# Performance work log

Measured on AMD Instinct MI355X. Metric: run time of the kernel, lower is better.

The kernel has to match this reference:

```python
import jax, jax.numpy as jnp
import numpy as np

B, C, H, W, IC = 8, 128, 64, 32, 64
NEG = -9.0e15  # matches torch's -9000000000000000.0 mask value


def setup_inputs() -> dict:
    key = jax.random.key(0)
    ks = jax.random.split(key, 8)
    x = jax.random.normal(ks[0], (B, C, H, W), dtype=jnp.float32)
    adj = jax.random.randint(ks[1], (H * W, H * W), 0, 2, dtype=jnp.int32)
    s = 0.1  # keep pre-softmax logits in a sane range
    g_w = jax.random.normal(ks[2], (IC, C), dtype=jnp.float32) * s
    theta_w = jax.random.normal(ks[3], (IC, C), dtype=jnp.float32) * s
    phi_w = jax.random.normal(ks[4], (IC, C), dtype=jnp.float32) * s
    cp_w = jax.random.normal(ks[5], (2 * IC,), dtype=jnp.float32) * s
    g_b = jnp.zeros((IC,), jnp.float32)
    theta_b = jnp.zeros((IC,), jnp.float32)
    phi_b = jnp.zeros((IC,), jnp.float32)
    return {"x": x, "adj": adj, "g_w": g_w, "g_b": g_b, "theta_w": theta_w,
            "theta_b": theta_b, "phi_w": phi_w, "phi_b": phi_b, "cp_w": cp_w}


def reference(x, adj, g_w, g_b, theta_w, theta_b, phi_w, phi_b, cp_w):
    b, c, h, w = x.shape
    n = h * w
    ic = g_w.shape[0]
    xf = x.reshape(b, c, n)  # flatten spatial sites: (B,C,N)
    # 1x1 convs == per-site linear projections
    g_x = jnp.einsum('oc,bcn->bno', g_w, xf) + g_b          # (B,N,IC)
    th = jnp.einsum('oc,bcn->bon', theta_w, xf) + theta_b[:, None]  # (B,IC,N)
    ph = jnp.einsum('oc,bcn->bon', phi_w, xf) + phi_b[:, None]      # (B,IC,N)
    # concat_project 1x1 conv on [theta;phi] channels == broadcast sum of two dot products
    w_t, w_p = cp_w[:ic], cp_w[ic:]
    f_t = jnp.einsum('o,bon->bn', w_t, th)  # (B,N)
    f_p = jnp.einsum('o,bon->bn', w_p, ph)  # (B,N)
    e = jax.nn.leaky_relu(f_t[:, :, None] + f_p[:, None, :], 0.2)  # (B,N,N)
    attention = jnp.where(adj > 0, jnp.float32(NEG), e)
    attention = jax.nn.softmax(attention, axis=-1)
    y = jnp.einsum('bij,bjo->bio', attention, g_x)  # (B,N,IC)
    return y.transpose(0, 2, 1).reshape(b, ic, h, w)
```

## Files before the change

### kernel.cpp

```cpp
#include <hip/hip_runtime.h>
#include <hip/hip_bf16.h>
#include <cstdint>

#define B_    8
#define C_    128
#define IC_   64
#define N_    2048
#define ROWS  16
#define LOG2E 1.44269504088896340736f

typedef __attribute__((ext_vector_type(8))) short bf16x8;
typedef __attribute__((ext_vector_type(4))) float f32x4;

#define OFF_FT   0
#define OFF_FP   16384
#define OFF_GXB  32768

static __device__ __forceinline__ ushort f2bf(float f) {
  __hip_bfloat16 h = __float2bfloat16(f);
  return *reinterpret_cast<ushort*>(&h);
}

__global__ __launch_bounds__(256) void k_gx(const float* __restrict__ x,
                                            const float* __restrict__ g_w,
                                            const float* __restrict__ g_b,
                                            const float* __restrict__ theta_w,
                                            const float* __restrict__ theta_b,
                                            const float* __restrict__ phi_w,
                                            const float* __restrict__ phi_b,
                                            const float* __restrict__ cp_w,
                                            float* __restrict__ ws) {
  __shared__ float xs[C_][64];
  __shared__ float wgT[C_][IC_];
  __shared__ float vtp[2][C_];
  __shared__ float fred[2][4][64];
  __shared__ float fb[2];
  int bx = blockIdx.x;
  int b = bx >> 5, n0 = (bx & 31) * 64;
  int t = threadIdx.x;

  const float* xb = x + (size_t)b * C_ * N_ + n0;
  for (int idx = t; idx < C_ * 64; idx += 256) {
    int c = idx >> 6, n = idx & 63;
    xs[c][n] = xb[(size_t)c * N_ + n];
  }
  for (int idx = t; idx < C_ * IC_; idx += 256) {
    int c = idx >> 6, o = idx & 63;
    wgT[c][o] = g_w[o * C_ + c];
  }
  {
    int half = t >> 7;
    int c = t & 127;
    const float* wmat = half ? phi_w : theta_w;
    const float* cw = cp_w + half * IC_;
    float a = 0.f;
#pragma unroll 8
    for (int o = 0; o < IC_; ++o) a += cw[o] * wmat[o * C_ + c];
    vtp[half][c] = a * LOG2E;
  }
  if (t < 2) {
    const float* bv = t ? phi_b : theta_b;
    const float* cw = cp_w + t * IC_;
    float a = 0.f;
    for (int o = 0; o < IC_; ++o) a += cw[o] * bv[o];
    fb[t] = a * LOG2E;
  }
  __syncthreads();

  int o4 = (t & 15) * 4, n4 = (t >> 4) * 4;
  float acc[4][4] = {};
#pragma unroll 4
  for (int c = 0; c < C_; ++c) {
    float4 xv = *(const float4*)&xs[c][n4];
    float4 wv = *(const float4*)&wgT[c][o4];
    acc[0][0] += wv.x * xv.x; acc[0][1] += wv.x * xv.y; acc[0][2] += wv.x * xv.z; acc[0][3] += wv.x * xv.w;
    acc[1][0] += wv.y * xv.x; acc[1][1] += wv.y * xv.y; acc[1][2] += wv.y * xv.z; acc[1][3] += wv.y * xv.w;
    acc[2][0] += wv.z * xv.x; acc[2][1] += wv.z * xv.y; acc[2][2] += wv.z * xv.z; acc[2][3] += wv.z * xv.w;
    acc[3][0] += wv.w * xv.x; acc[3][1] += wv.w * xv.y; acc[3][2] += wv.w * xv.z; acc[3][3] += wv.w * xv.w;
  }
  __hip_bfloat16* gxT = (__hip_bfloat16*)(ws + OFF_GXB) + (size_t)b * IC_ * N_;
#pragma unroll
  for (int oo = 0; oo < 4; ++oo) {
    float gb = g_b[o4 + oo];
    ushort4 pk = make_ushort4(f2bf(acc[oo][0] + gb), f2bf(acc[oo][1] + gb),
                              f2bf(acc[oo][2] + gb), f2bf(acc[oo][3] + gb));
    *(ushort4*)(gxT + (size_t)(o4 + oo) * N_ + n0 + n4) = pk;
  }

  {
    int n = t & 63, qr = t >> 6;
    float ft = 0.f, fp = 0.f;
#pragma unroll 8
    for (int cc = 0; cc < 32; ++cc) {
      int c = qr * 32 + cc;
      float xv = xs[c][n];
      ft += xv * vtp[0][c];
      fp += xv * vtp[1][c];
    }
    fred[0][qr][n] = ft;
    fred[1][qr][n] = fp;
  }
  __syncthreads();
  if (t < 128) {
    int n = t & 63, isp = t >> 6;
    float f = fb[isp] + fred[isp][0][n] + fred[isp][1][n]
            + fred[isp][2][n] + fred[isp][3][n];
    ws[(isp ? OFF_FP : OFF_FT) + b * N_ + n0 + n] = f;
  }
}

__global__ __launch_bounds__(256) void k_attn(const int* __restrict__ adj,
                                              const float* __restrict__ ws,
                                              float* __restrict__ out) {
  __shared__ char pbuf[2][ROWS * 512 * 2];
  __shared__ float rowsum[ROWS];

  int bx = blockIdx.x;
  int b = bx >> 7, tile = bx & 127;
  int i0 = tile * ROWS;
  int t = threadIdx.x;
  int w = t >> 6, lane = t & 63;
  int c16 = lane & 15, agrp = lane >> 4;

  const float* f_t = ws + OFF_FT + b * N_;
  const float4* fp4 = (const float4*)(ws + OFF_FP + b * N_);
  const __hip_bfloat16* gxT = (const __hip_bfloat16*)(ws + OFF_GXB) + (size_t)b * IC_ * N_;
  const __hip_bfloat16* gwav = gxT + (size_t)(w * 16 + c16) * N_ + agrp * 8;

  float fti[4];
#pragma unroll
  for (int rr = 0; rr < 4; ++rr) fti[rr] = f_t[i0 + w * 4 + rr];

  float rs[4] = {0.f, 0.f, 0.f, 0.f};
  f32x4 acc = {0.f, 0.f, 0.f, 0.f};

  for (int ch = 0; ch < 4; ++ch) {
    int j0 = ch * 512;
    char* pb = pbuf[ch & 1];
    float4 fa = fp4[j0 / 4 + lane * 2];
    float4 fbv = fp4[j0 / 4 + lane * 2 + 1];
#pragma unroll
    for (int rr = 0; rr < 4; ++rr) {
      int r = w * 4 + rr;
      const int4* ap = (const int4*)(adj + (size_t)(i0 + r) * N_ + j0) + lane * 2;
      int4 a0 = ap[0], a1 = ap[1];
      float ft = fti[rr];
      float s0 = ft + fa.x;  s0 = fmaxf(s0, 0.2f * s0);
      float s1 = ft + fa.y;  s1 = fmaxf(s1, 0.2f * s1);
      float s2 = ft + fa.z;  s2 = fmaxf(s2, 0.2f * s2);
      float s3 = ft + fa.w;  s3 = fmaxf(s3, 0.2f * s3);
      float s4 = ft + fbv.x; s4 = fmaxf(s4, 0.2f * s4);
      float s5 = ft + fbv.y; s5 = fmaxf(s5, 0.2f * s5);
      float s6 = ft + fbv.z; s6 = fmaxf(s6, 0.2f * s6);
      float s7 = ft + fbv.w; s7 = fmaxf(s7, 0.2f * s7);
      float p0 = (a0.x > 0) ? 0.f : exp2f(s0);
      float p1 = (a0.y > 0) ? 0.f : exp2f(s1);
      float p2 = (a0.z > 0) ? 0.f : exp2f(s2);
      float p3 = (a0.w > 0) ? 0.f : exp2f(s3);
      float p4 = (a1.x > 0) ? 0.f : exp2f(s4);
      float p5 = (a1.y > 0) ? 0.f : exp2f(s5);
      float p6 = (a1.z > 0) ? 0.f : exp2f(s6);
      float p7 = (a1.w > 0) ? 0.f : exp2f(s7);
      rs[rr] += ((p0 + p1) + (p2 + p3)) + ((p4 + p5) + (p6 + p7));
      bf16x8 pk;
      pk[0] = (short)f2bf(p0); pk[1] = (short)f2bf(p1);
      pk[2] = (short)f2bf(p2); pk[3] = (short)f2bf(p3);
      pk[4] = (short)f2bf(p4); pk[5] = (short)f2bf(p5);
      pk[6] = (short)f2bf(p6); pk[7] = (short)f2bf(p7);
      size_t byte = ((size_t)r * 1024 + (size_t)lane * 16) ^ ((size_t)(r & 7) << 4);
      *(bf16x8*)(pb + byte) = pk;
    }
    __syncthreads();
#pragma unroll
    for (int ks = 0; ks < 16; ++ks) {
      size_t ab = ((size_t)c16 * 1024 + (size_t)ks * 64 + (size_t)agrp * 16)
                ^ ((size_t)(c16 & 7) << 4);
      bf16x8 af = *(const bf16x8*)(pb + ab);
      bf16x8 bf = *(const bf16x8*)(gwav + j0 + ks * 32);
      acc = __builtin_amdgcn_mfma_f32_16x16x32_bf16(af, bf, acc, 0, 0, 0);
    }
  }

#pragma unroll
  for (int rr = 0; rr < 4; ++rr) {
    float s = rs[rr];
#pragma unroll
    for (int off = 32; off; off >>= 1) s += __shfl_xor(s, off, 64);
    if (lane == 0) rowsum[w * 4 + rr] = s;
  }
  __syncthreads();

  float4 rsv = *(const float4*)&rowsum[agrp * 4];
  float* op = out + ((size_t)b * IC_ + w * 16 + c16) * N_ + i0 + agrp * 4;
  float4 res = make_float4(acc[0] / rsv.x, acc[1] / rsv.y,
                           acc[2] / rsv.z, acc[3] / rsv.w);
  *(float4*)op = res;
}

extern "C" void kernel_launch(void* const* d_in, const int* in_sizes, int n_in,
                              void* d_out, int out_size, void* d_ws, size_t ws_size,
                              hipStream_t stream) {
  const float* x       = (const float*)d_in[0];
  const int*   adj     = (const int*)  d_in[1];
  const float* g_w     = (const float*)d_in[2];
  const float* g_b     = (const float*)d_in[3];
  const float* theta_w = (const float*)d_in[4];
  const float* theta_b = (const float*)d_in[5];
  const float* phi_w   = (const float*)d_in[6];
  const float* phi_b   = (const float*)d_in[7];
  const float* cp_w    = (const float*)d_in[8];
  float* out = (float*)d_out;
  float* ws  = (float*)d_ws;

  k_gx<<<B_ * (N_ / 64), 256, 0, stream>>>(x, g_w, g_b, theta_w, theta_b,
                                           phi_w, phi_b, cp_w, ws);
  k_attn<<<B_ * (N_ / ROWS), 256, 0, stream>>>(adj, ws, out);
}
```

Before: 133.6 us.

## Build attention MFMA operand in registers and retile rows per wave

```diff
diff --git a/kernel.cpp b/kernel.cpp
--- a/kernel.cpp
+++ b/kernel.cpp
@@ -6,7 +6,6 @@
 #define C_    128
 #define IC_   64
 #define N_    2048
-#define ROWS  16
 #define LOG2E 1.44269504088896340736f
 
 typedef __attribute__((ext_vector_type(8))) short bf16x8;
@@ -109,92 +108,80 @@
   }
 }
 
-__global__ __launch_bounds__(256) void k_attn(const int* __restrict__ adj,
-                                              const float* __restrict__ ws,
-                                              float* __restrict__ out) {
-  __shared__ char pbuf[2][ROWS * 512 * 2];
-  __shared__ float rowsum[ROWS];
-
+__global__ __launch_bounds__(256, 2) void k_attn(const int* __restrict__ adj,
+                                                 const float* __restrict__ ws,
+                                                 float* __restrict__ out) {
   int bx = blockIdx.x;
-  int b = bx >> 7, tile = bx & 127;
-  int i0 = tile * ROWS;
+  int b = bx >> 6, st = bx & 63;
   int t = threadIdx.x;
   int w = t >> 6, lane = t & 63;
-  int c16 = lane & 15, agrp = lane >> 4;
+  int col = lane & 15, agrp = lane >> 4;
+  int rowbase = st * 32 + (w >> 1) * 16;
+  int obase = (w & 1) * 32;
 
   const float* f_t = ws + OFF_FT + b * N_;
-  const float4* fp4 = (const float4*)(ws + OFF_FP + b * N_);
+  const float4* fpv = (const float4*)(ws + OFF_FP + b * N_);
   const __hip_bfloat16* gxT = (const __hip_bfloat16*)(ws + OFF_GXB) + (size_t)b * IC_ * N_;
-  const __hip_bfloat16* gwav = gxT + (size_t)(w * 16 + c16) * N_ + agrp * 8;
-
-  float fti[4];
-#pragma unroll
-  for (int rr = 0; rr < 4; ++rr) fti[rr] = f_t[i0 + w * 4 + rr];
-
-  float rs[4] = {0.f, 0.f, 0.f, 0.f};
-  f32x4 acc = {0.f, 0.f, 0.f, 0.f};
-
-  for (int ch = 0; ch < 4; ++ch) {
-    int j0 = ch * 512;
-    char* pb = pbuf[ch & 1];
-    float4 fa = fp4[j0 / 4 + lane * 2];
-    float4 fbv = fp4[j0 / 4 + lane * 2 + 1];
-#pragma unroll
-    for (int rr = 0; rr < 4; ++rr) {
-      int r = w * 4 + rr;
-      const int4* ap = (const int4*)(adj + (size_t)(i0 + r) * N_ + j0) + lane * 2;
-      int4 a0 = ap[0], a1 = ap[1];
-      float ft = fti[rr];
-      float s0 = ft + fa.x;  s0 = fmaxf(s0, 0.2f * s0);
-      float s1 = ft + fa.y;  s1 = fmaxf(s1, 0.2f * s1);
-      float s2 = ft + fa.z;  s2 = fmaxf(s2, 0.2f * s2);
-      float s3 = ft + fa.w;  s3 = fmaxf(s3, 0.2f * s3);
-      float s4 = ft + fbv.x; s4 = fmaxf(s4, 0.2f * s4);
-      float s5 = ft + fbv.y; s5 = fmaxf(s5, 0.2f * s5);
-      float s6 = ft + fbv.z; s6 = fmaxf(s6, 0.2f * s6);
-      float s7 = ft + fbv.w; s7 = fmaxf(s7, 0.2f * s7);
-      float p0 = (a0.x > 0) ? 0.f : exp2f(s0);
-      float p1 = (a0.y > 0) ? 0.f : exp2f(s1);
-      float p2 = (a0.z > 0) ? 0.f : exp2f(s2);
-      float p3 = (a0.w > 0) ? 0.f : exp2f(s3);
-      float p4 = (a1.x > 0) ? 0.f : exp2f(s4);
-      float p5 = (a1.y > 0) ? 0.f : exp2f(s5);
-      float p6 = (a1.z > 0) ? 0.f : exp2f(s6);
-      float p7 = (a1.w > 0) ? 0.f : exp2f(s7);
-      rs[rr] += ((p0 + p1) + (p2 + p3)) + ((p4 + p5) + (p6 + p7));
-      bf16x8 pk;
-      pk[0] = (short)f2bf(p0); pk[1] = (short)f2bf(p1);
-      pk[2] = (short)f2bf(p2); pk[3] = (short)f2bf(p3);
-      pk[4] = (short)f2bf(p4); pk[5] = (short)f2bf(p5);
-      pk[6] = (short)f2bf(p6); pk[7] = (short)f2bf(p7);
-      size_t byte = ((size_t)r * 1024 + (size_t)lane * 16) ^ ((size_t)(r & 7) << 4);
-      *(bf16x8*)(pb + byte) = pk;
-    }
-    __syncthreads();
-#pragma unroll
-    for (int ks = 0; ks < 16; ++ks) {
-      size_t ab = ((size_t)c16 * 1024 + (size_t)ks * 64 + (size_t)agrp * 16)
-                ^ ((size_t)(c16 & 7) << 4);
-      bf16x8 af = *(const bf16x8*)(pb + ab);
-      bf16x8 bf = *(const bf16x8*)(gwav + j0 + ks * 32);
-      acc = __builtin_amdgcn_mfma_f32_16x16x32_bf16(af, bf, acc, 0, 0, 0);
-    }
-  }
-
-#pragma unroll
-  for (int rr = 0; rr < 4; ++rr) {
-    float s = rs[rr];
-#pragma unroll
-    for (int off = 32; off; off >>= 1) s += __shfl_xor(s, off, 64);
-    if (lane == 0) rowsum[w * 4 + rr] = s;
-  }
-  __syncthreads();
-
-  float4 rsv = *(const float4*)&rowsum[agrp * 4];
-  float* op = out + ((size_t)b * IC_ + w * 16 + c16) * N_ + i0 + agrp * 4;
-  float4 res = make_float4(acc[0] / rsv.x, acc[1] / rsv.y,
-                           acc[2] / rsv.z, acc[3] / rsv.w);
-  *(float4*)op = res;
+  const __hip_bfloat16* gw0 = gxT + (size_t)(obase + col) * N_ + agrp * 8;
+  const __hip_bfloat16* gw1 = gw0 + 16 * N_;
+
+  float fti = f_t[rowbase + col];
+  const int4*   arow = (const int4*)(adj + (size_t)(rowbase + col) * N_) + agrp * 2;
+  const float4* fpl  = fpv + agrp * 2;
+
+  f32x4 acc0 = {0.f, 0.f, 0.f, 0.f};
+  f32x4 acc1 = {0.f, 0.f, 0.f, 0.f};
+  float rsum = 0.f;
+
+#pragma unroll 2
+  for (int ks = 0; ks < 64; ++ks) {
+    int4   a0 = arow[ks * 8];
+    int4   a1 = arow[ks * 8 + 1];
+    float4 f0 = fpl[ks * 8];
+    float4 f1 = fpl[ks * 8 + 1];
+    bf16x8 b0 = *(const bf16x8*)(gw0 + ks * 32);
+    bf16x8 b1 = *(const bf16x8*)(gw1 + ks * 32);
+
+    float s0 = fti + f0.x; s0 = fmaxf(s0, 0.2f * s0);
+    float s1 = fti + f0.y; s1 = fmaxf(s1, 0.2f * s1);
+    float s2 = fti + f0.z; s2 = fmaxf(s2, 0.2f * s2);
+    float s3 = fti + f0.w; s3 = fmaxf(s3, 0.2f * s3);
+    float s4 = fti + f1.x; s4 = fmaxf(s4, 0.2f * s4);
+    float s5 = fti + f1.y; s5 = fmaxf(s5, 0.2f * s5);
+    float s6 = fti + f1.z; s6 = fmaxf(s6, 0.2f * s6);
+    float s7 = fti + f1.w; s7 = fmaxf(s7, 0.2f * s7);
+    float p0 = (a0.x > 0) ? 0.f : exp2f(s0);
+    float p1 = (a0.y > 0) ? 0.f : exp2f(s1);
+    float p2 = (a0.z > 0) ? 0.f : exp2f(s2);
+    float p3 = (a0.w > 0) ? 0.f : exp2f(s3);
+    float p4 = (a1.x > 0) ? 0.f : exp2f(s4);
+    float p5 = (a1.y > 0) ? 0.f : exp2f(s5);
+    float p6 = (a1.z > 0) ? 0.f : exp2f(s6);
+    float p7 = (a1.w > 0) ? 0.f : exp2f(s7);
+    rsum += ((p0 + p1) + (p2 + p3)) + ((p4 + p5) + (p6 + p7));
+
+    bf16x8 af;
+    af[0] = (short)f2bf(p0); af[1] = (short)f2bf(p1);
+    af[2] = (short)f2bf(p2); af[3] = (short)f2bf(p3);
+    af[4] = (short)f2bf(p4); af[5] = (short)f2bf(p5);
+    af[6] = (short)f2bf(p6); af[7] = (short)f2bf(p7);
+
+    acc0 = __builtin_amdgcn_mfma_f32_16x16x32_bf16(af, b0, acc0, 0, 0, 0);
+    acc1 = __builtin_amdgcn_mfma_f32_16x16x32_bf16(af, b1, acc1, 0, 0, 0);
+  }
+
+  rsum += __shfl_xor(rsum, 16, 64);
+  rsum += __shfl_xor(rsum, 32, 64);
+  float r0 = __shfl(rsum, agrp * 4 + 0, 64);
+  float r1 = __shfl(rsum, agrp * 4 + 1, 64);
+  float r2 = __shfl(rsum, agrp * 4 + 2, 64);
+  float r3 = __shfl(rsum, agrp * 4 + 3, 64);
+
+  float4 res0 = make_float4(acc0[0] / r0, acc0[1] / r1, acc0[2] / r2, acc0[3] / r3);
+  float4 res1 = make_float4(acc1[0] / r0, acc1[1] / r1, acc1[2] / r2, acc1[3] / r3);
+  float* op = out + ((size_t)b * IC_ + obase + col) * N_ + rowbase + agrp * 4;
+  *(float4*)op             = res0;
+  *(float4*)(op + 16 * N_) = res1;
 }
 
 extern "C" void kernel_launch(void* const* d_in, const int* in_sizes, int n_in,
@@ -214,5 +201,5 @@
 
   k_gx<<<B_ * (N_ / 64), 256, 0, stream>>>(x, g_w, g_b, theta_w, theta_b,
                                            phi_w, phi_b, cp_w, ws);
-  k_attn<<<B_ * (N_ / ROWS), 256, 0, stream>>>(adj, ws, out);
-}
+  k_attn<<<B_ * (N_ / 32), 256, 0, stream>>>(adj, ws, out);
+}
```

Result: slower. 162.0 us (+21.2%).

## Split attention key range across waves with register prefetch and barrier-free LDS staging

Applied to the files above, without the earlier changes.

```diff
diff --git a/kernel.cpp b/kernel.cpp
--- a/kernel.cpp
+++ b/kernel.cpp
@@ -6,7 +6,6 @@
 #define C_    128
 #define IC_   64
 #define N_    2048
-#define ROWS  16
 #define LOG2E 1.44269504088896340736f
 
 typedef __attribute__((ext_vector_type(8))) short bf16x8;
@@ -109,92 +108,134 @@
   }
 }
 
-__global__ __launch_bounds__(256) void k_attn(const int* __restrict__ adj,
-                                              const float* __restrict__ ws,
-                                              float* __restrict__ out) {
-  __shared__ char pbuf[2][ROWS * 512 * 2];
-  __shared__ float rowsum[ROWS];
+__global__ __launch_bounds__(128, 2) void k_attn(const int* __restrict__ adj,
+                                                 const float* __restrict__ ws,
+                                                 float* __restrict__ out) {
+  __shared__ char pstage[2][2][2048];
+  __shared__ float mrg[64][20];
+  __shared__ float rsm[16];
 
   int bx = blockIdx.x;
-  int b = bx >> 7, tile = bx & 127;
-  int i0 = tile * ROWS;
+  int b = bx >> 7, rt = bx & 127;
+  int rowbase = rt * 16;
   int t = threadIdx.x;
-  int w = t >> 6, lane = t & 63;
-  int c16 = lane & 15, agrp = lane >> 4;
+  int wid = t >> 6, lane = t & 63;
+  int c16 = lane & 15, g8 = lane >> 4;
+  int jbase = wid * 1024;
 
   const float* f_t = ws + OFF_FT + b * N_;
-  const float4* fp4 = (const float4*)(ws + OFF_FP + b * N_);
+  const float* f_p = ws + OFF_FP + b * N_ + jbase + c16 * 4;
   const __hip_bfloat16* gxT = (const __hip_bfloat16*)(ws + OFF_GXB) + (size_t)b * IC_ * N_;
-  const __hip_bfloat16* gwav = gxT + (size_t)(w * 16 + c16) * N_ + agrp * 8;
 
   float fti[4];
 #pragma unroll
-  for (int rr = 0; rr < 4; ++rr) fti[rr] = f_t[i0 + w * 4 + rr];
-
-  float rs[4] = {0.f, 0.f, 0.f, 0.f};
-  f32x4 acc = {0.f, 0.f, 0.f, 0.f};
-
-  for (int ch = 0; ch < 4; ++ch) {
-    int j0 = ch * 512;
-    char* pb = pbuf[ch & 1];
-    float4 fa = fp4[j0 / 4 + lane * 2];
-    float4 fbv = fp4[j0 / 4 + lane * 2 + 1];
+  for (int rr = 0; rr < 4; ++rr) fti[rr] = f_t[rowbase + rr * 4 + g8];
+
+  const int* arow0 = adj + (size_t)(rowbase + g8) * N_ + jbase + c16 * 4;
+  const __hip_bfloat16* gw0 = gxT + (size_t)c16 * N_ + jbase + g8 * 8;
+
+  int4 ca[4]; float4 cf; bf16x8 cg[8];
+#pragma unroll
+  for (int rr = 0; rr < 4; ++rr) ca[rr] = *(const int4*)(arow0 + (size_t)rr * 4 * N_);
+  cf = *(const float4*)(f_p);
+#pragma unroll
+  for (int ot = 0; ot < 4; ++ot) {
+    cg[ot * 2 + 0] = *(const bf16x8*)(gw0 + (size_t)ot * 16 * N_);
+    cg[ot * 2 + 1] = *(const bf16x8*)(gw0 + (size_t)ot * 16 * N_ + 32);
+  }
+
+  f32x4 acc[4];
+#pragma unroll
+  for (int ot = 0; ot < 4; ++ot) acc[ot] = (f32x4){0.f, 0.f, 0.f, 0.f};
+  float rsum[4] = {0.f, 0.f, 0.f, 0.f};
+
+  for (int w = 0; w < 16; ++w) {
+    int nw = (w < 15) ? w + 1 : 15;
+    int4 na[4]; float4 nf; bf16x8 ng[8];
+#pragma unroll
+    for (int rr = 0; rr < 4; ++rr)
+      na[rr] = *(const int4*)(arow0 + (size_t)rr * 4 * N_ + nw * 64);
+    nf = *(const float4*)(f_p + nw * 64);
+#pragma unroll
+    for (int ot = 0; ot < 4; ++ot) {
+      ng[ot * 2 + 0] = *(const bf16x8*)(gw0 + (size_t)ot * 16 * N_ + nw * 64);
+      ng[ot * 2 + 1] = *(const bf16x8*)(gw0 + (size_t)ot * 16 * N_ + nw * 64 + 32);
+    }
+
+    char* pb = pstage[wid][w & 1];
 #pragma unroll
     for (int rr = 0; rr < 4; ++rr) {
-      int r = w * 4 + rr;
-      const int4* ap = (const int4*)(adj + (size_t)(i0 + r) * N_ + j0) + lane * 2;
-      int4 a0 = ap[0], a1 = ap[1];
+      int4 a = ca[rr];
       float ft = fti[rr];
-      float s0 = ft + fa.x;  s0 = fmaxf(s0, 0.2f * s0);
-      float s1 = ft + fa.y;  s1 = fmaxf(s1, 0.2f * s1);
-      float s2 = ft + fa.z;  s2 = fmaxf(s2, 0.2f * s2);
-      float s3 = ft + fa.w;  s3 = fmaxf(s3, 0.2f * s3);
-      float s4 = ft + fbv.x; s4 = fmaxf(s4, 0.2f * s4);
-      float s5 = ft + fbv.y; s5 = fmaxf(s5, 0.2f * s5);
-      float s6 = ft + fbv.z; s6 = fmaxf(s6, 0.2f * s6);
-      float s7 = ft + fbv.w; s7 = fmaxf(s7, 0.2f * s7);
-      float p0 = (a0.x > 0) ? 0.f : exp2f(s0);
-      float p1 = (a0.y > 0) ? 0.f : exp2f(s1);
-      float p2 = (a0.z > 0) ? 0.f : exp2f(s2);
-      float p3 = (a0.w > 0) ? 0.f : exp2f(s3);
-      float p4 = (a1.x > 0) ? 0.f : exp2f(s4);
-      float p5 = (a1.y > 0) ? 0.f : exp2f(s5);
-      float p6 = (a1.z > 0) ? 0.f : exp2f(s6);
-      float p7 = (a1.w > 0) ? 0.f : exp2f(s7);
-      rs[rr] += ((p0 + p1) + (p2 + p3)) + ((p4 + p5) + (p6 + p7));
-      bf16x8 pk;
-      pk[0] = (short)f2bf(p0); pk[1] = (short)f2bf(p1);
-      pk[2] = (short)f2bf(p2); pk[3] = (short)f2bf(p3);
-      pk[4] = (short)f2bf(p4); pk[5] = (short)f2bf(p5);
-      pk[6] = (short)f2bf(p6); pk[7] = (short)f2bf(p7);
-      size_t byte = ((size_t)r * 1024 + (size_t)lane * 16) ^ ((size_t)(r & 7) << 4);
-      *(bf16x8*)(pb + byte) = pk;
-    }
-    __syncthreads();
-#pragma unroll
-    for (int ks = 0; ks < 16; ++ks) {
-      size_t ab = ((size_t)c16 * 1024 + (size_t)ks * 64 + (size_t)agrp * 16)
-                ^ ((size_t)(c16 & 7) << 4);
-      bf16x8 af = *(const bf16x8*)(pb + ab);
-      bf16x8 bf = *(const bf16x8*)(gwav + j0 + ks * 32);
-      acc = __builtin_amdgcn_mfma_f32_16x16x32_bf16(af, bf, acc, 0, 0, 0);
-    }
+      float s0 = ft + cf.x; s0 = fmaxf(s0, 0.2f * s0);
+      float s1 = ft + cf.y; s1 = fmaxf(s1, 0.2f * s1);
+      float s2 = ft + cf.z; s2 = fmaxf(s2, 0.2f * s2);
+      float s3 = ft + cf.w; s3 = fmaxf(s3, 0.2f * s3);
+      float p0 = (a.x > 0) ? 0.f : exp2f(s0);
+      float p1 = (a.y > 0) ? 0.f : exp2f(s1);
+      float p2 = (a.z > 0) ? 0.f : exp2f(s2);
+      float p3 = (a.w > 0) ? 0.f : exp2f(s3);
+      rsum[rr] += (p0 + p1) + (p2 + p3);
+      ushort4 pk = make_ushort4(f2bf(p0), f2bf(p1), f2bf(p2), f2bf(p3));
+      int row = rr * 4 + g8;
+      int byte = (row * 128 + c16 * 8) ^ ((row & 7) << 4);
+      *(ushort4*)(pb + byte) = pk;
+    }
+
+#pragma unroll
+    for (int ks = 0; ks < 2; ++ks) {
+      int rbyte = (c16 * 128 + ks * 64 + g8 * 16) ^ ((c16 & 7) << 4);
+      bf16x8 af = *(const bf16x8*)(pb + rbyte);
+      acc[0] = __builtin_amdgcn_mfma_f32_16x16x32_bf16(af, cg[0 * 2 + ks], acc[0], 0, 0, 0);
+      acc[1] = __builtin_amdgcn_mfma_f32_16x16x32_bf16(af, cg[1 * 2 + ks], acc[1], 0, 0, 0);
+      acc[2] = __builtin_amdgcn_mfma_f32_16x16x32_bf16(af, cg[2 * 2 + ks], acc[2], 0, 0, 0);
+      acc[3] = __builtin_amdgcn_mfma_f32_16x16x32_bf16(af, cg[3 * 2 + ks], acc[3], 0, 0, 0);
+    }
+
+#pragma unroll
+    for (int rr = 0; rr < 4; ++rr) ca[rr] = na[rr];
+    cf = nf;
+#pragma unroll
+    for (int i = 0; i < 8; ++i) cg[i] = ng[i];
   }
 
 #pragma unroll
   for (int rr = 0; rr < 4; ++rr) {
-    float s = rs[rr];
-#pragma unroll
-    for (int off = 32; off; off >>= 1) s += __shfl_xor(s, off, 64);
-    if (lane == 0) rowsum[w * 4 + rr] = s;
+    rsum[rr] += __shfl_xor(rsum[rr], 1, 64);
+    rsum[rr] += __shfl_xor(rsum[rr], 2, 64);
+    rsum[rr] += __shfl_xor(rsum[rr], 4, 64);
+    rsum[rr] += __shfl_xor(rsum[rr], 8, 64);
+  }
+
+  if (wid == 1) {
+#pragma unroll
+    for (int ot = 0; ot < 4; ++ot) *(f32x4*)&mrg[lane][ot * 4] = acc[ot];
+    *(f32x4*)&mrg[lane][16] = (f32x4){rsum[0], rsum[1], rsum[2], rsum[3]};
   }
   __syncthreads();
-
-  float4 rsv = *(const float4*)&rowsum[agrp * 4];
-  float* op = out + ((size_t)b * IC_ + w * 16 + c16) * N_ + i0 + agrp * 4;
-  float4 res = make_float4(acc[0] / rsv.x, acc[1] / rsv.y,
-                           acc[2] / rsv.z, acc[3] / rsv.w);
-  *(float4*)op = res;
+  if (wid == 0) {
+#pragma unroll
+    for (int ot = 0; ot < 4; ++ot) {
+      f32x4 o1 = *(const f32x4*)&mrg[lane][ot * 4];
+      acc[ot][0] += o1[0]; acc[ot][1] += o1[1];
+      acc[ot][2] += o1[2]; acc[ot][3] += o1[3];
+    }
+    f32x4 r1 = *(const f32x4*)&mrg[lane][16];
+    rsum[0] += r1[0]; rsum[1] += r1[1]; rsum[2] += r1[2]; rsum[3] += r1[3];
+
+    if (c16 == 0) {
+      rsm[0 * 4 + g8] = rsum[0]; rsm[1 * 4 + g8] = rsum[1];
+      rsm[2 * 4 + g8] = rsum[2]; rsm[3 * 4 + g8] = rsum[3];
+    }
+    float4 rs4 = *(const float4*)&rsm[g8 * 4];
+
+#pragma unroll
+    for (int ot = 0; ot < 4; ++ot) {
+      float* op = out + ((size_t)b * IC_ + ot * 16 + c16) * N_ + rowbase + g8 * 4;
+      *(float4*)op = make_float4(acc[ot][0] / rs4.x, acc[ot][1] / rs4.y,
+                                 acc[ot][2] / rs4.z, acc[ot][3] / rs4.w);
+    }
+  }
 }
 
 extern "C" void kernel_launch(void* const* d_in, const int* in_sizes, int n_in,
@@ -214,5 +255,5 @@
 
   k_gx<<<B_ * (N_ / 64), 256, 0, stream>>>(x, g_w, g_b, theta_w, theta_b,
                                            phi_w, phi_b, cp_w, ws);
-  k_attn<<<B_ * (N_ / ROWS), 256, 0, stream>>>(adj, ws, out);
-}
+  k_attn<<<B_ * (N_ / 16), 128, 0, stream>>>(adj, ws, out);
+}
```

Result: faster. 130.8 us (-2.1%).
